# Optimization experiments

Measured on AMD Instinct MI355X. Metric: run time of the kernel, lower is better.

Reference implementation:

```python
import jax, jax.numpy as jnp
import numpy as np

D_MODEL = 1024
N_HEADS = 16
HEAD_DIM = D_MODEL // N_HEADS


def setup_inputs() -> dict:
    key = jax.random.key(0)
    kx, kq, kk, kv, ko = jax.random.split(key, 5)
    scale = 1.0 / np.sqrt(D_MODEL)
    x = jax.random.normal(kx, (4, 2048, D_MODEL), dtype=jnp.float32)
    # nn.Linear weights stored as [out, in]; y = x @ W.T
    W_q = jax.random.normal(kq, (D_MODEL, D_MODEL), dtype=jnp.float32) * scale
    W_k = jax.random.normal(kk, (D_MODEL, D_MODEL), dtype=jnp.float32) * scale
    W_v = jax.random.normal(kv, (D_MODEL, D_MODEL), dtype=jnp.float32) * scale
    W_o = jax.random.normal(ko, (D_MODEL, D_MODEL), dtype=jnp.float32) * scale
    return {"x": x, "W_q": W_q, "W_k": W_k, "W_v": W_v, "W_o": W_o}


def reference(x, W_q, W_k, W_v, W_o):
    B, T, C = x.shape
    H, Dh = N_HEADS, HEAD_DIM

    def proj(W):
        return (x @ W.T).reshape(B, T, H, Dh).transpose(0, 2, 1, 3)  # [B,H,T,Dh]

    Q = proj(W_q)
    K = proj(W_q)  # faithful to source bug: K uses W_q, W_k is unused
    V = proj(W_v)

    scores = jnp.einsum('bhqd,bhkd->bhqk', Q, K) / np.sqrt(Dh)
    causal = jnp.tril(jnp.ones((T, T), dtype=bool))
    scores = jnp.where(causal, scores, -jnp.inf)
    attn = jax.nn.softmax(scores, axis=-1)
    out = jnp.einsum('bhqk,bhkd->bhqd', attn, V)
    out = out.transpose(0, 2, 1, 3).reshape(B, T, C)
    return out @ W_o.T
```

## Files before the change

kernel.cpp:

```cpp
#include <hip/hip_runtime.h>
#include <hip/hip_bf16.h>
#include <type_traits>

typedef unsigned short u16;
typedef __attribute__((ext_vector_type(8))) short bf16x8;
typedef __attribute__((ext_vector_type(4))) float f32x4;

#define B_  4
#define T_  2048
#define C_  1024
#define H_  16
#define DH_ 64
#define M_  (B_*T_)

#define GLDS16(g, l) __builtin_amdgcn_global_load_lds( \
    (const __attribute__((address_space(1))) void*)(g), \
    (__attribute__((address_space(3))) void*)(l), 16, 0, 0)

__device__ __forceinline__ u16 f2b(float f) {
  union { __hip_bfloat16 h; u16 u; } cv;
  cv.h = __float2bfloat16(f);
  return cv.u;
}

__global__ void cast_all_kernel(const float* __restrict__ x,  const float* __restrict__ w0,
                                const float* __restrict__ w1, const float* __restrict__ w2,
                                u16* __restrict__ xo, u16* __restrict__ o0,
                                u16* __restrict__ o1, u16* __restrict__ o2) {
  int bid = blockIdx.x;
  const float* src; u16* dst; int blk;
  if (bid < 8192) { src = x; dst = xo; blk = bid; }
  else {
    int k = bid - 8192, w = k >> 10;
    src = (w == 0) ? w0 : (w == 1) ? w1 : w2;
    dst = (w == 0) ? o0 : (w == 1) ? o1 : o2;
    blk = k & 1023;
  }
  int i = (blk * 256 + threadIdx.x) * 4;
  float4 v = *(const float4*)(src + i);
  unsigned lo = (unsigned)f2b(v.x) | ((unsigned)f2b(v.y) << 16);
  unsigned hi = (unsigned)f2b(v.z) | ((unsigned)f2b(v.w) << 16);
  uint2 p; p.x = lo; p.y = hi;
  *(uint2*)(dst + i) = p;
}

__global__ __launch_bounds__(256) void gemm_bt_kernel(
    const u16* __restrict__ A, const u16* __restrict__ Bm,
    void* __restrict__ Cout, int mode)
{
  constexpr int K = 1024;
  __shared__ __align__(16) u16 As[128 * 64];
  __shared__ __align__(16) u16 Bs[128 * 64];

  const int tid  = threadIdx.x;
  const int wave = tid >> 6, lane = tid & 63;
  const int quad = lane >> 4, l15 = lane & 15;
  const int x7   = l15 & 7;
  const int wm = (wave >> 1) * 64, wn = (wave & 1) * 64;
  const int tm = blockIdx.x * 128, tn = blockIdx.y * 128;

  f32x4 acc[4][4] = {};

  for (int k0 = 0; k0 < K; k0 += 64) {
#pragma unroll
    for (int it = 0; it < 4; it++) {
      int ch  = it * 256 + tid;
      int row = ch >> 3;
      int cc  = (ch & 7) ^ (row & 7);
      GLDS16(A  + (size_t)(tm + row) * K + k0 + cc * 8, &As[(it * 256 + wave * 64) * 8]);
      GLDS16(Bm + (size_t)(tn + row) * K + k0 + cc * 8, &Bs[(it * 256 + wave * 64) * 8]);
    }
    __syncthreads();

#pragma unroll
    for (int ks = 0; ks < 2; ks++) {
      bf16x8 af[4], bfr[4];
#pragma unroll
      for (int t = 0; t < 4; t++) {
        int co = ((ks * 4 + quad) ^ x7) * 8;
        af[t]  = *(const bf16x8*)(&As[(wm + t * 16 + l15) * 64 + co]);
        bfr[t] = *(const bf16x8*)(&Bs[(wn + t * 16 + l15) * 64 + co]);
      }
#pragma unroll
      for (int mt = 0; mt < 4; mt++)
#pragma unroll
        for (int nt = 0; nt < 4; nt++)
          acc[mt][nt] = __builtin_amdgcn_mfma_f32_16x16x32_bf16(af[mt], bfr[nt], acc[mt][nt], 0, 0, 0);
    }
    __syncthreads();
  }

  if (mode == 0) {
    u16* out = (u16*)Cout;
    if (tn < 1024) {
#pragma unroll
      for (int mt = 0; mt < 4; mt++)
#pragma unroll
        for (int nt = 0; nt < 4; nt++)
#pragma unroll
          for (int r = 0; r < 4; r++) {
            int gm = tm + wm + mt * 16 + quad * 4 + r;
            int gn = tn + wn + nt * 16 + l15;
            int b = gm >> 11, t = gm & 2047;
            int h = gn >> 6, d = gn & 63;
            out[((size_t)((b * 16 + h) * 2048 + t) << 6) + d] = f2b(acc[mt][nt][r]);
          }
    } else {
#pragma unroll
      for (int mt = 0; mt < 4; mt++)
#pragma unroll
        for (int nt = 0; nt < 4; nt++) {
          int gm0 = tm + wm + mt * 16 + quad * 4;
          int gn  = tn - 1024 + wn + nt * 16 + l15;
          int b = gm0 >> 11, t0 = gm0 & 2047;
          int h = gn >> 6, d = gn & 63;
          alignas(8) u16 tmp[4];
#pragma unroll
          for (int r = 0; r < 4; r++) tmp[r] = f2b(acc[mt][nt][r]);
          *(ushort4*)(out + 8388608 + (((size_t)(b * 16 + h) * 64 + d) << 11) + t0)
              = *(const ushort4*)tmp;
        }
    }
  } else {
    float* out = (float*)Cout;
#pragma unroll
    for (int mt = 0; mt < 4; mt++)
#pragma unroll
      for (int nt = 0; nt < 4; nt++)
#pragma unroll
        for (int r = 0; r < 4; r++) {
          int gm = tm + wm + mt * 16 + quad * 4 + r;
          int gn = tn + wn + nt * 16 + l15;
          out[(size_t)gm * 1024 + gn] = acc[mt][nt][r];
        }
  }
}

__global__ __launch_bounds__(512, 4) void gemm_bt512_kernel(
    const u16* __restrict__ A, const u16* __restrict__ Bm, float* __restrict__ out)
{
  constexpr int K = 1024;
  __shared__ __align__(16) u16 As[128 * 64];
  __shared__ __align__(16) u16 Bs[128 * 64];

  const int tid  = threadIdx.x;
  const int wave = tid >> 6, lane = tid & 63;
  const int quad = lane >> 4, l15 = lane & 15;
  const int x7   = l15 & 7;
  const int wm = (wave >> 1) * 32, wn = (wave & 1) * 64;
  const int tm = blockIdx.x * 128, tn = blockIdx.y * 128;

  f32x4 acc[2][4] = {};

  for (int k0 = 0; k0 < K; k0 += 64) {
#pragma unroll
    for (int it = 0; it < 2; it++) {
      int ch  = it * 512 + tid;
      int row = ch >> 3;
      int cc  = (ch & 7) ^ (row & 7);
      GLDS16(A  + (size_t)(tm + row) * K + k0 + cc * 8, &As[(it * 512 + wave * 64) * 8]);
      GLDS16(Bm + (size_t)(tn + row) * K + k0 + cc * 8, &Bs[(it * 512 + wave * 64) * 8]);
    }
    __syncthreads();

#pragma unroll
    for (int ks = 0; ks < 2; ks++) {
      bf16x8 af[2], bfr[4];
      int co = ((ks * 4 + quad) ^ x7) * 8;
#pragma unroll
      for (int t = 0; t < 2; t++)
        af[t]  = *(const bf16x8*)(&As[(wm + t * 16 + l15) * 64 + co]);
#pragma unroll
      for (int t = 0; t < 4; t++)
        bfr[t] = *(const bf16x8*)(&Bs[(wn + t * 16 + l15) * 64 + co]);
#pragma unroll
      for (int mt = 0; mt < 2; mt++)
#pragma unroll
        for (int nt = 0; nt < 4; nt++)
          acc[mt][nt] = __builtin_amdgcn_mfma_f32_16x16x32_bf16(af[mt], bfr[nt], acc[mt][nt], 0, 0, 0);
    }
    __syncthreads();
  }

#pragma unroll
  for (int mt = 0; mt < 2; mt++)
#pragma unroll
    for (int nt = 0; nt < 4; nt++)
#pragma unroll
      for (int r = 0; r < 4; r++) {
        int gm = tm + wm + mt * 16 + quad * 4 + r;
        int gn = tn + wn + nt * 16 + l15;
        out[(size_t)gm * 1024 + gn] = acc[mt][nt][r];
      }
}

__global__ __launch_bounds__(256, 4) void attn_kernel(
    const u16* __restrict__ Q, const u16* __restrict__ Vt, u16* __restrict__ AO)
{
  constexpr int LDP = 72;
  __shared__ __align__(16) u16 Ks[4096];
  __shared__ __align__(16) u16 Vs[4096];
  __shared__ __align__(16) u16 Ps[4][32 * LDP];

  const int tid  = threadIdx.x;
  const int wave = tid >> 6, lane = tid & 63;
  const int quad = lane >> 4, l15 = lane & 15;
  const int x7   = l15 & 7;
  const int bid  = blockIdx.x;
  const int bh = (bid & 7) * 8 + ((bid >> 3) & 7);
  const int m  = bid >> 6;
  const int i  = (m & 4) ? ((m & 8) ? m - 12 : m + 4) : 15 - m;
  const int b = bh >> 4, h = bh & 15;
  const u16* Qbh = Q  + (size_t)bh * (T_ * DH_);
  const u16* Vbh = Vt + (size_t)bh * (DH_ * T_);
  const int q0w = i * 128 + wave * 32;
  const int kbd = (q0w + 31) >> 6;
  const int nkb = 2 * i + 2;
  u16* myP = &Ps[wave][0];

  const float C1 = 0.18033688f;
  const float C2 = -28.8539008f;
  const bf16x8 ones = { 0x3F80, 0x3F80, 0x3F80, 0x3F80, 0x3F80, 0x3F80, 0x3F80, 0x3F80 };

  bf16x8 qf[2][2];
#pragma unroll
  for (int mt = 0; mt < 2; mt++)
#pragma unroll
    for (int ks = 0; ks < 2; ks++)
      qf[mt][ks] = *(const bf16x8*)(Qbh + (size_t)(q0w + mt * 16 + l15) * DH_ + ks * 32 + quad * 8);

  f32x4 o[2][4] = {};
  f32x4 lsumv[2] = {};

  auto tilecomp = [&](int kb, auto DIAGC) {
    constexpr bool DIAG = decltype(DIAGC)::value;
    const int k0 = kb * 64;
    f32x4 s[2][4] = {};
#pragma unroll
    for (int ks = 0; ks < 2; ks++)
#pragma unroll
      for (int nt = 0; nt < 4; nt++) {
        bf16x8 kf = *(const bf16x8*)(&Ks[(nt * 16 + l15) * 64 + (((ks * 4 + quad) ^ x7) * 8)]);
#pragma unroll
        for (int mt = 0; mt < 2; mt++)
          s[mt][nt] = __builtin_amdgcn_mfma_f32_16x16x32_bf16(qf[mt][ks], kf, s[mt][nt], 0, 0, 0);
      }

#pragma unroll
    for (int mt = 0; mt < 2; mt++)
#pragma unroll
      for (int nt = 0; nt < 4; nt++)
#pragma unroll
        for (int r = 0; r < 4; r++) {
          float p = __builtin_amdgcn_exp2f(s[mt][nt][r] * C1 + C2);
          if constexpr (DIAG) {
            int qg = q0w + mt * 16 + quad * 4 + r;
            int kg = k0 + nt * 16 + l15;
            p = (kg <= qg) ? p : 0.0f;
          }
          myP[(mt * 16 + quad * 4 + r) * LDP + nt * 16 + l15] = f2b(p);
        }

#pragma unroll
    for (int ks2 = 0; ks2 < 2; ks2++) {
      bf16x8 pf[2];
#pragma unroll
      for (int mt = 0; mt < 2; mt++) {
        pf[mt] = *(const bf16x8*)(&myP[(mt * 16 + l15) * LDP + ks2 * 32 + quad * 8]);
        lsumv[mt] = __builtin_amdgcn_mfma_f32_16x16x32_bf16(pf[mt], ones, lsumv[mt], 0, 0, 0);
      }
#pragma unroll
      for (int dt = 0; dt < 4; dt++) {
        bf16x8 vf = *(const bf16x8*)(&Vs[(dt * 16 + l15) * 64 + (((ks2 * 4 + quad) ^ x7) * 8)]);
#pragma unroll
        for (int mt = 0; mt < 2; mt++)
          o[mt][dt] = __builtin_amdgcn_mfma_f32_16x16x32_bf16(pf[mt], vf, o[mt][dt], 0, 0, 0);
      }
    }
  };

  for (int kb = 0; kb < nkb; kb++) {
    const int k0 = kb * 64;
#pragma unroll
    for (int it = 0; it < 2; it++) {
      int ch  = it * 256 + tid;
      int row = ch >> 3;
      int cc  = (ch & 7) ^ (row & 7);
      GLDS16(Qbh + (size_t)(k0 + row) * DH_ + cc * 8, &Ks[(it * 256 + wave * 64) * 8]);
      GLDS16(Vbh + (size_t)row * T_ + k0 + cc * 8,    &Vs[(it * 256 + wave * 64) * 8]);
    }
    __syncthreads();

    if (kb < kbd)        tilecomp(kb, std::false_type{});
    else if (kb == kbd)  tilecomp(kb, std::true_type{});
    __syncthreads();
  }

#pragma unroll
  for (int mt = 0; mt < 2; mt++)
#pragma unroll
    for (int r = 0; r < 4; r++) {
      float rl = 1.0f / lsumv[mt][r];
      int t = q0w + mt * 16 + quad * 4 + r;
#pragma unroll
      for (int dt = 0; dt < 4; dt++)
        AO[((size_t)(b * T_ + t)) * C_ + h * DH_ + dt * 16 + l15] = f2b(o[mt][dt][r] * rl);
    }
}

extern "C" void kernel_launch(void* const* d_in, const int* in_sizes, int n_in,
                              void* d_out, int out_size, void* d_ws, size_t ws_size,
                              hipStream_t stream) {
  (void)in_sizes; (void)n_in; (void)out_size; (void)ws_size;
  const float* x  = (const float*)d_in[0];
  const float* Wq = (const float*)d_in[1];
  const float* Wv = (const float*)d_in[3];
  const float* Wo = (const float*)d_in[4];

  u16* Xb  = (u16*)d_ws;
  u16* AOw = Xb;
  u16* Wqb = Xb  + 8388608;
  u16* Wvb = Wqb + 1048576;
  u16* Wob = Wvb + 1048576;
  u16* Qw  = Wob + 1048576;
  u16* Vtw = Qw  + 8388608;

  cast_all_kernel<<<11264, 256, 0, stream>>>(x, Wq, Wv, Wo, Xb, Wqb, Wvb, Wob);

  gemm_bt_kernel<<<dim3(64, 16), 256, 0, stream>>>(Xb, Wqb, (void*)Qw, 0);

  attn_kernel<<<1024, 256, 0, stream>>>(Qw, Vtw, AOw);

  gemm_bt512_kernel<<<dim3(64, 8), 512, 0, stream>>>(AOw, Wob, (float*)d_out);
}
```

Before: 222.6 us.

## Double-buffer K/V tiles and keep P in registers via permlane swaps

K and V LDS tiles are now double-buffered, so the next block's global-to-LDS loads are issued before computing the current block. This leaves one barrier per iteration instead of two. The QK^T MFMA operands are swapped so S comes out transposed, with a permuted K row mapping. P is then packed into bf16 pairs and rearranged with permlane32_swap to form the A operand of the PV MFMA directly. This removes the per-wave P scratch buffer and its LDS write/read round trip, at the cost of extra cross-lane shuffles and a correctness risk in the mask and layout remapping.

```diff
diff --git a/kernel.cpp b/kernel.cpp
--- a/kernel.cpp
+++ b/kernel.cpp
@@ -5,6 +5,7 @@
 typedef unsigned short u16;
 typedef __attribute__((ext_vector_type(8))) short bf16x8;
 typedef __attribute__((ext_vector_type(4))) float f32x4;
+typedef __attribute__((ext_vector_type(2))) unsigned int u32x2;
 
 #define B_  4
 #define T_  2048
@@ -197,15 +198,15 @@
 __global__ __launch_bounds__(256, 4) void attn_kernel(
     const u16* __restrict__ Q, const u16* __restrict__ Vt, u16* __restrict__ AO)
 {
-  constexpr int LDP = 72;
-  __shared__ __align__(16) u16 Ks[4096];
-  __shared__ __align__(16) u16 Vs[4096];
-  __shared__ __align__(16) u16 Ps[4][32 * LDP];
+  __shared__ __align__(16) u16 Ks[2][4096];
+  __shared__ __align__(16) u16 Vs[2][4096];
 
   const int tid  = threadIdx.x;
   const int wave = tid >> 6, lane = tid & 63;
   const int quad = lane >> 4, l15 = lane & 15;
   const int x7   = l15 & 7;
+  const int krow = (l15 & 3) | ((l15 & 4) << 1) | ((l15 & 8) >> 1);
+  const int kx7  = krow & 7;
   const int bid  = blockIdx.x;
   const int bh = (bid & 7) * 8 + ((bid >> 3) & 7);
   const int m  = bid >> 6;
@@ -216,84 +217,100 @@
   const int q0w = i * 128 + wave * 32;
   const int kbd = (q0w + 31) >> 6;
   const int nkb = 2 * i + 2;
-  u16* myP = &Ps[wave][0];
 
   const float C1 = 0.18033688f;
   const float C2 = -28.8539008f;
   const bf16x8 ones = { 0x3F80, 0x3F80, 0x3F80, 0x3F80, 0x3F80, 0x3F80, 0x3F80, 0x3F80 };
 
-  bf16x8 qf[2][2];
-#pragma unroll
-  for (int mt = 0; mt < 2; mt++)
-#pragma unroll
-    for (int ks = 0; ks < 2; ks++)
-      qf[mt][ks] = *(const bf16x8*)(Qbh + (size_t)(q0w + mt * 16 + l15) * DH_ + ks * 32 + quad * 8);
-
   f32x4 o[2][4] = {};
   f32x4 lsumv[2] = {};
 
-  auto tilecomp = [&](int kb, auto DIAGC) {
-    constexpr bool DIAG = decltype(DIAGC)::value;
-    const int k0 = kb * 64;
-    f32x4 s[2][4] = {};
-#pragma unroll
-    for (int ks = 0; ks < 2; ks++)
-#pragma unroll
-      for (int nt = 0; nt < 4; nt++) {
-        bf16x8 kf = *(const bf16x8*)(&Ks[(nt * 16 + l15) * 64 + (((ks * 4 + quad) ^ x7) * 8)]);
-#pragma unroll
-        for (int mt = 0; mt < 2; mt++)
-          s[mt][nt] = __builtin_amdgcn_mfma_f32_16x16x32_bf16(qf[mt][ks], kf, s[mt][nt], 0, 0, 0);
-      }
-
-#pragma unroll
-    for (int mt = 0; mt < 2; mt++)
-#pragma unroll
-      for (int nt = 0; nt < 4; nt++)
-#pragma unroll
-        for (int r = 0; r < 4; r++) {
-          float p = __builtin_amdgcn_exp2f(s[mt][nt][r] * C1 + C2);
-          if constexpr (DIAG) {
-            int qg = q0w + mt * 16 + quad * 4 + r;
-            int kg = k0 + nt * 16 + l15;
-            p = (kg <= qg) ? p : 0.0f;
-          }
-          myP[(mt * 16 + quad * 4 + r) * LDP + nt * 16 + l15] = f2b(p);
-        }
-
-#pragma unroll
-    for (int ks2 = 0; ks2 < 2; ks2++) {
-      bf16x8 pf[2];
-#pragma unroll
-      for (int mt = 0; mt < 2; mt++) {
-        pf[mt] = *(const bf16x8*)(&myP[(mt * 16 + l15) * LDP + ks2 * 32 + quad * 8]);
-        lsumv[mt] = __builtin_amdgcn_mfma_f32_16x16x32_bf16(pf[mt], ones, lsumv[mt], 0, 0, 0);
-      }
-#pragma unroll
-      for (int dt = 0; dt < 4; dt++) {
-        bf16x8 vf = *(const bf16x8*)(&Vs[(dt * 16 + l15) * 64 + (((ks2 * 4 + quad) ^ x7) * 8)]);
-#pragma unroll
-        for (int mt = 0; mt < 2; mt++)
-          o[mt][dt] = __builtin_amdgcn_mfma_f32_16x16x32_bf16(pf[mt], vf, o[mt][dt], 0, 0, 0);
-      }
-    }
-  };
-
-  for (int kb = 0; kb < nkb; kb++) {
+  auto stage = [&](int kb, int bufi) {
     const int k0 = kb * 64;
 #pragma unroll
     for (int it = 0; it < 2; it++) {
       int ch  = it * 256 + tid;
       int row = ch >> 3;
       int cc  = (ch & 7) ^ (row & 7);
-      GLDS16(Qbh + (size_t)(k0 + row) * DH_ + cc * 8, &Ks[(it * 256 + wave * 64) * 8]);
-      GLDS16(Vbh + (size_t)row * T_ + k0 + cc * 8,    &Vs[(it * 256 + wave * 64) * 8]);
-    }
-    __syncthreads();
-
-    if (kb < kbd)        tilecomp(kb, std::false_type{});
-    else if (kb == kbd)  tilecomp(kb, std::true_type{});
-    __syncthreads();
+      GLDS16(Qbh + (size_t)(k0 + row) * DH_ + cc * 8, &Ks[bufi][(it * 256 + wave * 64) * 8]);
+      GLDS16(Vbh + (size_t)row * T_ + k0 + cc * 8,    &Vs[bufi][(it * 256 + wave * 64) * 8]);
+    }
+  };
+
+  stage(0, 0);
+
+  bf16x8 qf[2][2];
+#pragma unroll
+  for (int mt = 0; mt < 2; mt++)
+#pragma unroll
+    for (int ks = 0; ks < 2; ks++)
+      qf[mt][ks] = *(const bf16x8*)(Qbh + (size_t)(q0w + mt * 16 + l15) * DH_ + ks * 32 + quad * 8);
+
+  auto tilecomp = [&](int kb, int bufi, auto DIAGC) {
+    constexpr bool DIAG = decltype(DIAGC)::value;
+    const int k0 = kb * 64;
+    const u16* KsB = Ks[bufi];
+    const u16* VsB = Vs[bufi];
+
+    f32x4 s[2][4] = {};
+#pragma unroll
+    for (int ks = 0; ks < 2; ks++)
+#pragma unroll
+      for (int nt = 0; nt < 4; nt++) {
+        bf16x8 kf = *(const bf16x8*)(&KsB[(nt * 16 + krow) * 64 + (((ks * 4 + quad) ^ kx7) * 8)]);
+#pragma unroll
+        for (int mt = 0; mt < 2; mt++)
+          s[mt][nt] = __builtin_amdgcn_mfma_f32_16x16x32_bf16(kf, qf[mt][ks], s[mt][nt], 0, 0, 0);
+      }
+
+    unsigned c[2][4][2];
+#pragma unroll
+    for (int mt = 0; mt < 2; mt++)
+#pragma unroll
+      for (int nt = 0; nt < 4; nt++) {
+        u16 pb[4];
+#pragma unroll
+        for (int r = 0; r < 4; r++) {
+          float p = __builtin_amdgcn_exp2f(s[mt][nt][r] * C1 + C2);
+          if constexpr (DIAG) {
+            int qg = q0w + mt * 16 + l15;
+            int kg = k0 + nt * 16 + (quad & 1) * 8 + (quad >> 1) * 4 + r;
+            p = (kg <= qg) ? p : 0.0f;
+          }
+          pb[r] = f2b(p);
+        }
+        c[mt][nt][0] = (unsigned)pb[0] | ((unsigned)pb[1] << 16);
+        c[mt][nt][1] = (unsigned)pb[2] | ((unsigned)pb[3] << 16);
+      }
+
+#pragma unroll
+    for (int ks2 = 0; ks2 < 2; ks2++) {
+      bf16x8 pf[2];
+#pragma unroll
+      for (int mt = 0; mt < 2; mt++) {
+        u32x2 w02 = __builtin_amdgcn_permlane32_swap(c[mt][2 * ks2][0], c[mt][2 * ks2 + 1][0], false, false);
+        u32x2 w13 = __builtin_amdgcn_permlane32_swap(c[mt][2 * ks2][1], c[mt][2 * ks2 + 1][1], false, false);
+        union { unsigned u[4]; bf16x8 v; } pk;
+        pk.u[0] = w02[0]; pk.u[1] = w13[0]; pk.u[2] = w02[1]; pk.u[3] = w13[1];
+        pf[mt] = pk.v;
+        lsumv[mt] = __builtin_amdgcn_mfma_f32_16x16x32_bf16(pf[mt], ones, lsumv[mt], 0, 0, 0);
+      }
+#pragma unroll
+      for (int dt = 0; dt < 4; dt++) {
+        bf16x8 vf = *(const bf16x8*)(&VsB[(dt * 16 + l15) * 64 + (((ks2 * 4 + quad) ^ x7) * 8)]);
+#pragma unroll
+        for (int mt = 0; mt < 2; mt++)
+          o[mt][dt] = __builtin_amdgcn_mfma_f32_16x16x32_bf16(pf[mt], vf, o[mt][dt], 0, 0, 0);
+      }
+    }
+  };
+
+  for (int kb = 0; kb < nkb; kb++) {
+    __syncthreads();
+    if (kb + 1 < nkb) stage(kb + 1, (kb + 1) & 1);
+    const int bufi = kb & 1;
+    if (kb < kbd)        tilecomp(kb, bufi, std::false_type{});
+    else if (kb == kbd)  tilecomp(kb, bufi, std::true_type{});
   }
 
 #pragma unroll
```

After: 210.3 us. 5.5% less time.
